# Performance work log

Measured on AMD Instinct MI355X. Metric: run time of the kernel, lower is better.

Reference implementation:

```python
import jax, jax.numpy as jnp
import numpy as np

GAMMA = 0.05      # train_config['loss']['gamma']
WARP = 256.0      # train_config['loss']['warp']
LAMBDA = 2.0      # train_config['loss']['lambda']
KL_START = 2000
KL_END = 8000
KL_UPPER = 1.0
BIG = 1e8  # stand-in for +inf that keeps softmin gradients finite


def kl_anneal(step):
    if step < KL_START:
        return 0.0
    elif step >= KL_END:
        return KL_UPPER
    else:
        return KL_UPPER * ((step - KL_START) / (KL_END - KL_START))


def _soft_dtw(x, y, gamma, warp):
    """Batched soft-DTW with warp penalty, anti-diagonal wavefront scan.
    x: (B, N, C), y: (B, M, C). Returns (B,) alignment costs R[N, M]."""
    B, N, C = x.shape
    M = y.shape[1]
    # squared Euclidean pairwise distance via GEMM (no (B,N,M,C) intermediate)
    x2 = jnp.sum(x * x, -1)
    y2 = jnp.sum(y * y, -1)
    D = x2[:, :, None] + y2[:, None, :] - 2.0 * jnp.einsum('bnc,bmc->bnm', x, y)  # (B,N,M)

    # precompute anti-diagonals of D: d = i + j runs 2..N+M, i runs 1..N, j = d - i
    ds = jnp.arange(2, N + M + 1)                      # (ND,) ND = N+M-1
    ii = jnp.arange(1, N + 1)                          # (N,)
    jj = ds[:, None] - ii[None, :]                     # (ND, N)
    valid = (jj >= 1) & (jj <= M)                      # (ND, N)
    Dg = D[:, (ii - 1)[None, :], jnp.clip(jj - 1, 0, M - 1)]  # (B, ND, N)
    Dg = jnp.where(valid[None], Dg, 0.0)
    Dg = jnp.transpose(Dg, (1, 0, 2))                  # (ND, B, N)

    # carry two previous R diagonals, each indexed by i = 0..N
    two = jnp.full((B, N + 1), BIG, x.dtype).at[:, 0].set(0.0)  # d = 0: R[0,0] = 0
    one = jnp.full((B, N + 1), BIG, x.dtype)                    # d = 1: all inf
    big_col = jnp.full((B, 1), BIG, x.dtype)

    def step(carry, inp):
        two, one = carry
        Dd, vld = inp                      # (B, N), (N,)
        diag = two[:, :-1]                 # R[i-1, j-1]
        up = one[:, :-1] + warp            # R[i-1, j] + warp
        left = one[:, 1:] + warp           # R[i, j-1] + warp
        s = jnp.stack([diag, up, left], 0)
        sm = -gamma * jax.nn.logsumexp(-s / gamma, axis=0)  # soft-min
        row = jnp.where(vld[None, :], Dd + sm, BIG)          # i = 1..N
        new = jnp.concatenate([big_col, row], axis=1)        # i = 0 row is inf
        return (one, new), None

    (_, last), _ = jax.lax.scan(step, (two, one), (Dg, valid))
    return last[:, N]  # R[N, M]


def setup_inputs() -> dict:
    key = jax.random.key(0)
    ks = jax.random.split(key, 7)
    K, B, T, C, S, Z = 4, 8, 800, 80, 128, 32
    return {
        "mel_iters": jax.random.normal(ks[0], (K, B, T, C), jnp.float32),
        "mel_targets": jax.random.normal(ks[1], (B, T, C), jnp.float32),
        "mel_lens_targets": jax.random.randint(ks[2], (B,), 100, T, jnp.int32),
        "src_lens_targets": jax.random.randint(ks[3], (B,), 50, S, jnp.int32),
        "durations": jax.random.uniform(ks[4], (B, S), jnp.float32, 0.0, 6.0),
        "mus": jax.random.normal(ks[5], (B, Z), jnp.float32),
        "log_vars": jax.random.normal(ks[6], (B, Z), jnp.float32),
        "step": 5000,
    }


def reference(mel_iters, mel_targets, mel_lens_targets, src_lens_targets,
              durations, mus, log_vars, step):
    K, B, T, C = mel_iters.shape
    y = jax.nn.sigmoid(mel_targets)                       # (B, T, C)
    xs = jax.nn.sigmoid(mel_iters).reshape(K * B, T, C)
    ys = jnp.broadcast_to(y[None], (K, B, T, C)).reshape(K * B, T, C)
    d = _soft_dtw(xs, ys, GAMMA, WARP).reshape(K, B)      # (K, B)
    # torch: mel_iter_loss += sdtw(...).mean()  (scalar sum of per-iter batch means)
    mel_iter_loss = jnp.sum(jnp.mean(d, axis=1))
    mel_lens_f = mel_lens_targets.astype(jnp.float32)
    mel_loss = jnp.mean(mel_iter_loss / (K * mel_lens_f))

    dur_err = jnp.abs(jnp.sum(durations, -1) - mel_lens_f)
    duration_loss = LAMBDA * jnp.mean(dur_err / src_lens_targets.astype(jnp.float32))

    beta = jnp.asarray(kl_anneal(step), jnp.float32)
    kl_loss = -0.5 * jnp.sum(1.0 + log_vars - mus ** 2 - jnp.exp(log_vars))

    total_loss = mel_loss + duration_loss + beta * kl_loss
    return (total_loss, mel_loss, duration_loss, kl_loss, beta)
```

## Files before the change

### kernel.cpp

```cpp
#include <hip/hip_runtime.h>
#include <math.h>
#include <stdint.h>

constexpr int K_ = 4, B_ = 8, T_ = 800, C_ = 80, S_ = 128, Z_ = 32;
constexpr int KB_ = K_ * B_;
constexpr int TC_ = T_ * C_;

#define BIGV   1e8f
#define WARP_V 256.0f

constexpr int NU_   = 900;
constexpr int SLAB_ = NU_ * 800;

__device__ __forceinline__ float sigmoidf_(float v) {
    return 1.f / (1.f + __expf(-v));
}

__global__ void fill_edge(float* __restrict__ Dm) {
    int kb = blockIdx.x;
    int t = threadIdx.x;
    if (t < 184) {
        int i = 8 + t;
        Dm[(size_t)kb * SLAB_ + (size_t)((i >> 3) - 1) * 800 + i] = BIGV;
    }
}

__global__ __launch_bounds__(256) void gemm_band(const float* __restrict__ mel_iters,
                                                 const float* __restrict__ mel_targets,
                                                 float* __restrict__ Dm) {
    const int kb = blockIdx.z;
    const int b  = kb & 7;
    const int ti = blockIdx.y;
    const int tj = ti + (int)blockIdx.x - 2;
    if ((unsigned)tj > 12u) return;

    const float* __restrict__ Xb = mel_iters + (size_t)kb * TC_;
    const float* __restrict__ Yb = mel_targets + (size_t)b * TC_;

    __shared__ float smem[10880];
    __shared__ float x2s[64], y2s[64];
    float (*xa)[68] = (float(*)[68])smem;
    float (*ya)[68] = (float(*)[68])(smem + 5440);

    const int tid = threadIdx.x;
    const int tx = tid & 15, ty = tid >> 4;
    const int i0 = ti * 64, j0 = tj * 64;

    {
        const int row = tid & 63, seg = tid >> 6;
        const int gi = min(i0 + row, T_ - 1);
        const int gj = min(j0 + row, T_ - 1);
        const float4* Xr = (const float4*)(Xb + (size_t)gi * C_);
        const float4* Yr = (const float4*)(Yb + (size_t)gj * C_);
        #pragma unroll
        for (int m = 0; m < 5; ++m) {
            const int k4 = seg * 5 + m;
            float4 xv = Xr[k4], yv = Yr[k4];
            const int k = k4 * 4;
            xa[k + 0][row] = sigmoidf_(xv.x); xa[k + 1][row] = sigmoidf_(xv.y);
            xa[k + 2][row] = sigmoidf_(xv.z); xa[k + 3][row] = sigmoidf_(xv.w);
            ya[k + 0][row] = sigmoidf_(yv.x); ya[k + 1][row] = sigmoidf_(yv.y);
            ya[k + 2][row] = sigmoidf_(yv.z); ya[k + 3][row] = sigmoidf_(yv.w);
        }
    }
    __syncthreads();

    if (tid < 64) {
        float s = 0.f;
        for (int k = 0; k < C_; ++k) { float v = xa[k][tid]; s += v * v; }
        x2s[tid] = s;
    } else if (tid < 128) {
        float s = 0.f;
        for (int k = 0; k < C_; ++k) { float v = ya[k][tid - 64]; s += v * v; }
        y2s[tid - 64] = s;
    }

    float acc[4][4] = {};
    #pragma unroll 16
    for (int k = 0; k < C_; ++k) {
        float4 av = *(const float4*)&xa[k][ty * 4];
        float4 bv = *(const float4*)&ya[k][tx * 4];
        acc[0][0] += av.x * bv.x; acc[0][1] += av.x * bv.y; acc[0][2] += av.x * bv.z; acc[0][3] += av.x * bv.w;
        acc[1][0] += av.y * bv.x; acc[1][1] += av.y * bv.y; acc[1][2] += av.y * bv.z; acc[1][3] += av.y * bv.w;
        acc[2][0] += av.z * bv.x; acc[2][1] += av.z * bv.y; acc[2][2] += av.z * bv.z; acc[2][3] += av.z * bv.w;
        acc[3][0] += av.w * bv.x; acc[3][1] += av.w * bv.y; acc[3][2] += av.w * bv.z; acc[3][3] += av.w * bv.w;
    }
    __syncthreads();

    float xs2[4], ys2[4];
    #pragma unroll
    for (int r = 0; r < 4; ++r) xs2[r] = x2s[ty * 4 + r];
    #pragma unroll
    for (int c = 0; c < 4; ++c) ys2[c] = y2s[tx * 4 + c];

    float* Zt = smem;
    const int sb = ty >> 1;
    #pragma unroll
    for (int r = 0; r < 4; ++r)
        #pragma unroll
        for (int c = 0; c < 4; ++c)
            Zt[(4 * tx + c + sb) * 65 + (4 * ty + r)] = xs2[r] + ys2[c] - 2.f * acc[r][c];
    __syncthreads();

    const int w0 = tid >> 6;
    const int lane = tid & 63;
    const int iGlob = i0 + lane;
    const int sbl = lane >> 3;
    const bool iok = iGlob < T_;
    const size_t ub = (size_t)(j0 + 8 * ti) * 800 + iGlob;
    #pragma unroll
    for (int it = 0; it < 18; ++it) {
        int w = w0 + it * 4;
        if (w > 70) break;
        int jrel = w - sbl;
        if (iok && (unsigned)jrel < 64u && (j0 + jrel) < T_)
            Dm[(size_t)kb * SLAB_ + ub + (size_t)w * 800] = Zt[w * 65 + lane];
    }
}


#define DCELL2(aS,aA,aB,aC,aD,aW, bS,bA,bB,bC,bD,bW) \
  "v_min3_f32 v" #aS ", v" #aA ", v" #aB ", v" #aC "\n\t" \
  "v_min3_f32 v" #bS ", v" #bA ", v" #bB ", v" #bC "\n\t" \
  "v_add_f32 v" #aS ", v" #aS ", v" #aD "\n\t" \
  "v_add_f32 v" #bS ", v" #bS ", v" #bD "\n\t" \
  "v_add_f32 v" #aW ", %[wK], v" #aS "\n\t" \
  "v_add_f32 v" #bW ", %[wK], v" #bS "\n\t"

#define STEP_E(q0,q1,q2,q3,q4,q5,q6,q7,q8,q9,q10,q11,q12,q13,q14,q15) \
  DCELL2(82, 45, 48, 66, q0, 98,    90, 89, 73, 74, q8, 106) \
  DCELL2(83, 50, 98, 67, q1, 99,    91, 58, 106, 75, q9, 107) \
  DCELL2(84, 51, 99, 68, q2, 100,   92, 59, 107, 76, q10, 108) \
  DCELL2(85, 52, 100, 69, q3, 101,  93, 60, 108, 77, q11, 109) \
  DCELL2(86, 53, 101, 70, q4, 102,  94, 61, 109, 78, q12, 110) \
  DCELL2(87, 54, 102, 71, q5, 103,  95, 62, 110, 79, q13, 111) \
  DCELL2(88, 55, 103, 72, q6, 104,  96, 63, 111, 80, q14, 112) \
  DCELL2(89, 56, 104, 73, q7, 105,  97, 64, 112, 81, q15, 113)

#define STEP_O(q0,q1,q2,q3,q4,q5,q6,q7,q8,q9,q10,q11,q12,q13,q14,q15) \
  DCELL2(50, 47, 46, 98, q0, 66,    58, 57, 105, 106, q8, 74) \
  DCELL2(51, 82, 66, 99, q1, 67,    59, 90, 74, 107, q9, 75) \
  DCELL2(52, 83, 67, 100, q2, 68,   60, 91, 75, 108, q10, 76) \
  DCELL2(53, 84, 68, 101, q3, 69,   61, 92, 76, 109, q11, 77) \
  DCELL2(54, 85, 69, 102, q4, 70,   62, 93, 77, 110, q12, 78) \
  DCELL2(55, 86, 70, 103, q5, 71,   63, 94, 78, 111, q13, 79) \
  DCELL2(56, 87, 71, 104, q6, 72,   64, 95, 79, 112, q14, 80) \
  DCELL2(57, 88, 72, 105, q7, 73,   65, 96, 80, 113, q15, 81)

#define HO_E \
  "s_nop 1\n\t" \
  "v_mov_b32_dpp v43, v97 wave_shr:1 row_mask:0xf bank_mask:0xf bound_ctrl:0\n\t" \
  "v_cndmask_b32 v45, v43, v42, %[msk]\n\t" \
  "v_add_f32 v46, %[wK], v45\n\t"

#define HO_O \
  "s_nop 1\n\t" \
  "v_mov_b32_dpp v43, v65 wave_shr:1 row_mask:0xf bank_mask:0xf bound_ctrl:0\n\t" \
  "v_cndmask_b32 v47, v43, v42, %[msk]\n\t" \
  "v_add_f32 v48, %[wK], v47\n\t"

#define PREF(r0,r1,r2,r3,K) \
  "s_add_u32 %[st], %[su], " #K "\n\t" \
  "v_med3_i32 v43, %[st], %[vlo], %[vhi]\n\t" \
  "v_mad_u32_u24 v44, v43, %[c32], %[vl4]\n\t" \
  "global_load_dwordx4 " r0 ", v44, %[bp]\n\t" \
  "global_load_dwordx4 " r1 ", v44, %[bp] offset:16\n\t" \
  "global_load_dwordx4 " r2 ", v44, %[bp] offset:32\n\t" \
  "global_load_dwordx4 " r3 ", v44, %[bp] offset:48\n\t"

#define PREF0(K) PREF("v[114:117]","v[118:121]","v[122:125]","v[126:129]",K)
#define PREF1(K) PREF("v[130:133]","v[134:137]","v[138:141]","v[142:145]",K)
#define PREF2(K) PREF("v[146:149]","v[150:153]","v[154:157]","v[158:161]",K)
#define PREF3(K) PREF("v[162:165]","v[166:169]","v[170:173]","v[174:177]",K)
#define PREF4(K) PREF("v[178:181]","v[182:185]","v[186:189]","v[190:193]",K)
#define PREF5(K) PREF("v[194:197]","v[198:201]","v[202:205]","v[206:209]",K)
#define PREF6(K) PREF("v[210:213]","v[214:217]","v[218:221]","v[222:225]",K)
#define PREF7(K) PREF("v[226:229]","v[230:233]","v[234:237]","v[238:241]",K)

#define SLOT0 (114,115,116,117,118,119,120,121,122,123,124,125,126,127,128,129)
#define SLOT1 (130,131,132,133,134,135,136,137,138,139,140,141,142,143,144,145)
#define SLOT2 (146,147,148,149,150,151,152,153,154,155,156,157,158,159,160,161)
#define SLOT3 (162,163,164,165,166,167,168,169,170,171,172,173,174,175,176,177)
#define SLOT4 (178,179,180,181,182,183,184,185,186,187,188,189,190,191,192,193)
#define SLOT5 (194,195,196,197,198,199,200,201,202,203,204,205,206,207,208,209)
#define SLOT6 (210,211,212,213,214,215,216,217,218,219,220,221,222,223,224,225)
#define SLOT7 (226,227,228,229,230,231,232,233,234,235,236,237,238,239,240,241)

#define DTW_CALL(M, A) M A

#define MV(n) "v_mov_b32 v" #n ", v42\n\t"
#define W28 "s_waitcnt vmcnt(28)\n\t"

__global__ __launch_bounds__(64)
void dtw_wave_kernel(const float* __restrict__ Dm, float* __restrict__ dtwv) {
    const int kb = blockIdx.x;
    const int l  = threadIdx.x;
    const int lc = l < 49 ? l : 49;
    const float* __restrict__ Dd = Dm + (size_t)kb * SLAB_;

    const int ti_l = lc >> 2;
    const int Jlo = ti_l >= 2 ? 64 * (ti_l - 2) : 0;
    const int Jhi = min(799, 64 * ti_l + 191);
    const int lo_u = (Jlo == 0) ? (2 * lc) : (Jlo + 2 * lc + 1);
    const int hi_u = Jhi + 2 * lc + 1;
    const unsigned lofs4 = (unsigned)(lc << 6);

    float res;
    unsigned su_d, st_d;

    asm volatile(
        "v_mov_b32 v42, %[vbig]\n\t"
        MV(50) MV(51) MV(52) MV(53) MV(54) MV(55) MV(56) MV(57)
        MV(58) MV(59) MV(60) MV(61) MV(62) MV(63) MV(64) MV(65)
        MV(66) MV(67) MV(68) MV(69) MV(70) MV(71) MV(72) MV(73)
        MV(74) MV(75) MV(76) MV(77) MV(78) MV(79) MV(80) MV(81)
        MV(82) MV(83) MV(84) MV(85) MV(86) MV(87) MV(88) MV(89)
        MV(90) MV(91) MV(92) MV(93) MV(94) MV(95) MV(96) MV(97)
        MV(98) MV(99) MV(100) MV(101) MV(102) MV(103) MV(104) MV(105)
        MV(106) MV(107) MV(108) MV(109) MV(110) MV(111) MV(112) MV(113)
        "v_cndmask_b32 v45, v42, 0, %[msk]\n\t"
        "v_mov_b32 v46, v42\n\t"
        "v_mov_b32 v47, v42\n\t"
        "v_mov_b32 v48, v42\n\t"
        "s_mov_b32 %[su], 0\n\t"
        PREF0(0) PREF1(1) PREF2(2) PREF3(3) PREF4(4) PREF5(5) PREF6(6) PREF7(7)
        "1:\n\t"
        W28 DTW_CALL(STEP_E, SLOT0) HO_E PREF0(8)
        W28 DTW_CALL(STEP_O, SLOT1) HO_O PREF1(9)
        W28 DTW_CALL(STEP_E, SLOT2) HO_E PREF2(10)
        W28 DTW_CALL(STEP_O, SLOT3) HO_O PREF3(11)
        W28 DTW_CALL(STEP_E, SLOT4) HO_E PREF4(12)
        W28 DTW_CALL(STEP_O, SLOT5) HO_O PREF5(13)
        W28 DTW_CALL(STEP_E, SLOT6) HO_E PREF6(14)
        W28 DTW_CALL(STEP_O, SLOT7) HO_O PREF7(15)
        "s_add_u32 %[su], %[su], 8\n\t"
        "s_cmp_lg_u32 %[su], 888\n\t"
        "s_cbranch_scc1 1b\n\t"
        W28 DTW_CALL(STEP_E, SLOT0) HO_E PREF0(8)
        W28 DTW_CALL(STEP_O, SLOT1) HO_O PREF1(9)
        W28 DTW_CALL(STEP_E, SLOT2) HO_E PREF2(10)
        W28 DTW_CALL(STEP_O, SLOT3) HO_O
        "s_waitcnt vmcnt(24)\n\t" DTW_CALL(STEP_E, SLOT4) HO_E
        "s_waitcnt vmcnt(20)\n\t" DTW_CALL(STEP_O, SLOT5) HO_O
        "s_waitcnt vmcnt(16)\n\t" DTW_CALL(STEP_E, SLOT6) HO_E
        "s_waitcnt vmcnt(12)\n\t" DTW_CALL(STEP_O, SLOT7) HO_O
        "s_waitcnt vmcnt(8)\n\t"  DTW_CALL(STEP_E, SLOT0) HO_E
        "s_waitcnt vmcnt(4)\n\t"  DTW_CALL(STEP_O, SLOT1) HO_O
        "s_waitcnt vmcnt(0)\n\t"  DTW_CALL(STEP_E, SLOT2)
        "v_mov_b32 %[res], v97\n\t"
        : [res] "=v"(res), [su] "=&s"(su_d), [st] "=&s"(st_d)
        : [vlo] "v"(lo_u), [vhi] "v"(hi_u), [vl4] "v"(lofs4),
          [vbig] "v"(BIGV), [wK] "s"(WARP_V), [c32] "s"(3200u),
          [msk] "s"(1ull), [bp] "s"((const void*)Dd)
        : "memory", "scc",
          "v42","v43","v44","v45","v46","v47","v48","v49",
          "v50","v51","v52","v53","v54","v55","v56","v57","v58","v59",
          "v60","v61","v62","v63","v64","v65","v66","v67","v68","v69",
          "v70","v71","v72","v73","v74","v75","v76","v77","v78","v79",
          "v80","v81","v82","v83","v84","v85","v86","v87","v88","v89",
          "v90","v91","v92","v93","v94","v95","v96","v97","v98","v99",
          "v100","v101","v102","v103","v104","v105","v106","v107","v108","v109",
          "v110","v111","v112","v113","v114","v115","v116","v117","v118","v119",
          "v120","v121","v122","v123","v124","v125","v126","v127","v128","v129",
          "v130","v131","v132","v133","v134","v135","v136","v137","v138","v139",
          "v140","v141","v142","v143","v144","v145","v146","v147","v148","v149",
          "v150","v151","v152","v153","v154","v155","v156","v157","v158","v159",
          "v160","v161","v162","v163","v164","v165","v166","v167","v168","v169",
          "v170","v171","v172","v173","v174","v175","v176","v177","v178","v179",
          "v180","v181","v182","v183","v184","v185","v186","v187","v188","v189",
          "v190","v191","v192","v193","v194","v195","v196","v197","v198","v199",
          "v200","v201","v202","v203","v204","v205","v206","v207","v208","v209",
          "v210","v211","v212","v213","v214","v215","v216","v217","v218","v219",
          "v220","v221","v222","v223","v224","v225","v226","v227","v228","v229",
          "v230","v231","v232","v233","v234","v235","v236","v237","v238","v239",
          "v240","v241"
    );

    if (l == 49) dtwv[kb] = res;
}

__global__ void finalize_kernel(const float* __restrict__ dtwv, const int* __restrict__ mel_lens,
                                const int* __restrict__ src_lens, const float* __restrict__ durations,
                                const float* __restrict__ mus, const float* __restrict__ log_vars,
                                const int* __restrict__ step, float* __restrict__ out) {
    const int lane = threadIdx.x;

    float v = (lane < KB_) ? dtwv[lane] : 0.f;
    for (int o = 32; o; o >>= 1) v += __shfl_down(v, o);

    float w = (lane < B_) ? 1.f / (K_ * (float)mel_lens[lane]) : 0.f;
    for (int o = 32; o; o >>= 1) w += __shfl_down(w, o);

    float du = 0.f;
    if (lane < B_) {
        float s = 0.f;
        for (int j = 0; j < S_; ++j) s += durations[lane * S_ + j];
        du = fabsf(s - (float)mel_lens[lane]) / (float)src_lens[lane];
    }
    for (int o = 32; o; o >>= 1) du += __shfl_down(du, o);

    float kl = 0.f;
    for (int j = lane; j < B_ * Z_; j += 64) {
        float muv = mus[j], lv = log_vars[j];
        kl += 1.f + lv - muv * muv - expf(lv);
    }
    for (int o = 32; o; o >>= 1) kl += __shfl_down(kl, o);

    if (lane == 0) {
        float mel_iter_loss = v / (float)B_;
        float mel_loss = mel_iter_loss * (w / (float)B_);
        float dur_loss = 2.0f * du / (float)B_;
        float kl_loss = -0.5f * kl;
        int st = step[0];
        float beta = (st < 2000) ? 0.f : ((st >= 8000) ? 1.f : (float)(st - 2000) / 6000.f);
        out[0] = mel_loss + dur_loss + beta * kl_loss;
        out[1] = mel_loss;
        out[2] = dur_loss;
        out[3] = kl_loss;
        out[4] = beta;
    }
}

extern "C" void kernel_launch(void* const* d_in, const int* in_sizes, int n_in,
                              void* d_out, int out_size, void* d_ws, size_t ws_size,
                              hipStream_t stream) {
    const float* mel_iters   = (const float*)d_in[0];
    const float* mel_targets = (const float*)d_in[1];
    const int*   mel_lens    = (const int*)d_in[2];
    const int*   src_lens    = (const int*)d_in[3];
    const float* durations   = (const float*)d_in[4];
    const float* mus         = (const float*)d_in[5];
    const float* log_vars    = (const float*)d_in[6];
    const int*   step        = (const int*)d_in[7];
    float* out = (float*)d_out;

    float* ws   = (float*)d_ws;
    float* Dm   = ws;
    float* dtwv = Dm + (size_t)KB_ * SLAB_;

    fill_edge<<<KB_, 192, 0, stream>>>(Dm);

    gemm_band<<<dim3(5, 13, KB_), 256, 0, stream>>>(mel_iters, mel_targets, Dm);

    dtw_wave_kernel<<<KB_, 64, 0, stream>>>(Dm, dtwv);

    finalize_kernel<<<1, 64, 0, stream>>>(dtwv, mel_lens, src_lens, durations, mus, log_vars, step, out);
}
```

Measured before the change: 213.7 us.

## Change skewed DTW slab layout and regroup wavefront cells for more ILP

The skew of the precomputed distance slab changes so that lanes own rows offset by 4 per lane instead of 2. The slab grows to 999 steps, and the edge-fill and GEMM store indexing are rewritten to match. The DTW asm step now interleaves four independent cell chains instead of two. This is meant to hide the min3/add latency of the serial wavefront with more independent instructions. In exchange the scan runs more steps (984 vs 888 loop bound) and the slab footprint grows.

```diff
diff --git a/kernel.cpp b/kernel.cpp
--- a/kernel.cpp
+++ b/kernel.cpp
@@ -9,7 +9,7 @@
 #define BIGV   1e8f
 #define WARP_V 256.0f
 
-constexpr int NU_   = 900;
+constexpr int NU_   = 999;
 constexpr int SLAB_ = NU_ * 800;
 
 __device__ __forceinline__ float sigmoidf_(float v) {
@@ -18,10 +18,18 @@
 
 __global__ void fill_edge(float* __restrict__ Dm) {
     int kb = blockIdx.x;
-    int t = threadIdx.x;
-    if (t < 184) {
-        int i = 8 + t;
-        Dm[(size_t)kb * SLAB_ + (size_t)((i >> 3) - 1) * 800 + i] = BIGV;
+    #pragma unroll
+    for (int m = 0; m < 5; ++m) {
+        int idx = threadIdx.x + 256 * m;
+        if (idx >= 1200) break;
+        int blk = idx / 24, rem = idx % 24;
+        int row, k;
+        if (rem < 4)       { row = 4 + rem;                 k = 1; }
+        else if (rem < 12) { int e = rem - 4;  row = 8 + (e >> 1);  k = 1 + (e & 1); }
+        else               { int e = rem - 12; row = 12 + e / 3;    k = 1 + e % 3; }
+        int i = 16 * blk + row;
+        int u = 4 * blk + (row >> 2) - k;
+        Dm[(size_t)kb * SLAB_ + (size_t)u * 800 + i] = BIGV;
     }
 }
 
@@ -94,7 +102,7 @@
     for (int c = 0; c < 4; ++c) ys2[c] = y2s[tx * 4 + c];
 
     float* Zt = smem;
-    const int sb = ty >> 1;
+    const int sb = ty;
     #pragma unroll
     for (int r = 0; r < 4; ++r)
         #pragma unroll
@@ -105,13 +113,13 @@
     const int w0 = tid >> 6;
     const int lane = tid & 63;
     const int iGlob = i0 + lane;
-    const int sbl = lane >> 3;
+    const int sbl = lane >> 2;
     const bool iok = iGlob < T_;
-    const size_t ub = (size_t)(j0 + 8 * ti) * 800 + iGlob;
-    #pragma unroll
-    for (int it = 0; it < 18; ++it) {
+    const size_t ub = (size_t)(j0 + 16 * ti) * 800 + iGlob;
+    #pragma unroll
+    for (int it = 0; it < 20; ++it) {
         int w = w0 + it * 4;
-        if (w > 70) break;
+        if (w > 78) break;
         int jrel = w - sbl;
         if (iok && (unsigned)jrel < 64u && (j0 + jrel) < T_)
             Dm[(size_t)kb * SLAB_ + ub + (size_t)w * 800] = Zt[w * 65 + lane];
@@ -119,33 +127,31 @@
 }
 
 
-#define DCELL2(aS,aA,aB,aC,aD,aW, bS,bA,bB,bC,bD,bW) \
-  "v_min3_f32 v" #aS ", v" #aA ", v" #aB ", v" #aC "\n\t" \
-  "v_min3_f32 v" #bS ", v" #bA ", v" #bB ", v" #bC "\n\t" \
-  "v_add_f32 v" #aS ", v" #aS ", v" #aD "\n\t" \
-  "v_add_f32 v" #bS ", v" #bS ", v" #bD "\n\t" \
-  "v_add_f32 v" #aW ", %[wK], v" #aS "\n\t" \
-  "v_add_f32 v" #bW ", %[wK], v" #bS "\n\t"
+#define QUAD(s0,w0,d0,u0,l0,q0, s1,w1,d1,u1,l1,q1, s2,w2,d2,u2,l2,q2, s3,w3,d3,u3,l3,q3) \
+  "v_min3_f32 v" #s0 ", v" #d0 ", v" #u0 ", v" #l0 "\n\t" \
+  "v_min3_f32 v" #s1 ", v" #d1 ", v" #u1 ", v" #l1 "\n\t" \
+  "v_min3_f32 v" #s2 ", v" #d2 ", v" #u2 ", v" #l2 "\n\t" \
+  "v_min3_f32 v" #s3 ", v" #d3 ", v" #u3 ", v" #l3 "\n\t" \
+  "v_add_f32 v" #s0 ", v" #s0 ", v" #q0 "\n\t" \
+  "v_add_f32 v" #s1 ", v" #s1 ", v" #q1 "\n\t" \
+  "v_add_f32 v" #s2 ", v" #s2 ", v" #q2 "\n\t" \
+  "v_add_f32 v" #s3 ", v" #s3 ", v" #q3 "\n\t" \
+  "v_add_f32 v" #w0 ", %[wK], v" #s0 "\n\t" \
+  "v_add_f32 v" #w1 ", %[wK], v" #s1 "\n\t" \
+  "v_add_f32 v" #w2 ", %[wK], v" #s2 "\n\t" \
+  "v_add_f32 v" #w3 ", %[wK], v" #s3 "\n\t"
 
 #define STEP_E(q0,q1,q2,q3,q4,q5,q6,q7,q8,q9,q10,q11,q12,q13,q14,q15) \
-  DCELL2(82, 45, 48, 66, q0, 98,    90, 89, 73, 74, q8, 106) \
-  DCELL2(83, 50, 98, 67, q1, 99,    91, 58, 106, 75, q9, 107) \
-  DCELL2(84, 51, 99, 68, q2, 100,   92, 59, 107, 76, q10, 108) \
-  DCELL2(85, 52, 100, 69, q3, 101,  93, 60, 108, 77, q11, 109) \
-  DCELL2(86, 53, 101, 70, q4, 102,  94, 61, 109, 78, q12, 110) \
-  DCELL2(87, 54, 102, 71, q5, 103,  95, 62, 110, 79, q13, 111) \
-  DCELL2(88, 55, 103, 72, q6, 104,  96, 63, 111, 80, q14, 112) \
-  DCELL2(89, 56, 104, 73, q7, 105,  97, 64, 112, 81, q15, 113)
+  QUAD(82,98,45,48,66,q0,    86,102,85,69,70,q4,   90,106,89,73,74,q8,   94,110,93,77,78,q12) \
+  QUAD(83,99,50,98,67,q1,    87,103,54,102,71,q5,  91,107,58,106,75,q9,  95,111,62,110,79,q13) \
+  QUAD(84,100,51,99,68,q2,   88,104,55,103,72,q6,  92,108,59,107,76,q10, 96,112,63,111,80,q14) \
+  QUAD(85,101,52,100,69,q3,  89,105,56,104,73,q7,  93,109,60,108,77,q11, 97,113,64,112,81,q15)
 
 #define STEP_O(q0,q1,q2,q3,q4,q5,q6,q7,q8,q9,q10,q11,q12,q13,q14,q15) \
-  DCELL2(50, 47, 46, 98, q0, 66,    58, 57, 105, 106, q8, 74) \
-  DCELL2(51, 82, 66, 99, q1, 67,    59, 90, 74, 107, q9, 75) \
-  DCELL2(52, 83, 67, 100, q2, 68,   60, 91, 75, 108, q10, 76) \
-  DCELL2(53, 84, 68, 101, q3, 69,   61, 92, 76, 109, q11, 77) \
-  DCELL2(54, 85, 69, 102, q4, 70,   62, 93, 77, 110, q12, 78) \
-  DCELL2(55, 86, 70, 103, q5, 71,   63, 94, 78, 111, q13, 79) \
-  DCELL2(56, 87, 71, 104, q6, 72,   64, 95, 79, 112, q14, 80) \
-  DCELL2(57, 88, 72, 105, q7, 73,   65, 96, 80, 113, q15, 81)
+  QUAD(50,66,47,46,98,q0,    54,70,53,101,102,q4,  58,74,57,105,106,q8,  62,78,61,109,110,q12) \
+  QUAD(51,67,82,66,99,q1,    55,71,86,70,103,q5,   59,75,90,74,107,q9,   63,79,94,78,111,q13) \
+  QUAD(52,68,83,67,100,q2,   56,72,87,71,104,q6,   60,76,91,75,108,q10,  64,80,95,79,112,q14) \
+  QUAD(53,69,84,68,101,q3,   57,73,88,72,105,q7,   61,77,92,76,109,q11,  65,81,96,80,113,q15)
 
 #define HO_E \
   "s_nop 1\n\t" \
@@ -201,8 +207,8 @@
     const int ti_l = lc >> 2;
     const int Jlo = ti_l >= 2 ? 64 * (ti_l - 2) : 0;
     const int Jhi = min(799, 64 * ti_l + 191);
-    const int lo_u = (Jlo == 0) ? (2 * lc) : (Jlo + 2 * lc + 1);
-    const int hi_u = Jhi + 2 * lc + 1;
+    const int lo_u = (Jlo == 0) ? (4 * lc) : (Jlo + 4 * lc + 3);
+    const int hi_u = min(998, Jhi + 4 * lc + 3);
     const unsigned lofs4 = (unsigned)(lc << 6);
 
     float res;
@@ -234,19 +240,23 @@
         W28 DTW_CALL(STEP_E, SLOT6) HO_E PREF6(14)
         W28 DTW_CALL(STEP_O, SLOT7) HO_O PREF7(15)
         "s_add_u32 %[su], %[su], 8\n\t"
-        "s_cmp_lg_u32 %[su], 888\n\t"
+        "s_cmp_lg_u32 %[su], 984\n\t"
         "s_cbranch_scc1 1b\n\t"
         W28 DTW_CALL(STEP_E, SLOT0) HO_E PREF0(8)
         W28 DTW_CALL(STEP_O, SLOT1) HO_O PREF1(9)
         W28 DTW_CALL(STEP_E, SLOT2) HO_E PREF2(10)
-        W28 DTW_CALL(STEP_O, SLOT3) HO_O
-        "s_waitcnt vmcnt(24)\n\t" DTW_CALL(STEP_E, SLOT4) HO_E
-        "s_waitcnt vmcnt(20)\n\t" DTW_CALL(STEP_O, SLOT5) HO_O
-        "s_waitcnt vmcnt(16)\n\t" DTW_CALL(STEP_E, SLOT6) HO_E
-        "s_waitcnt vmcnt(12)\n\t" DTW_CALL(STEP_O, SLOT7) HO_O
-        "s_waitcnt vmcnt(8)\n\t"  DTW_CALL(STEP_E, SLOT0) HO_E
-        "s_waitcnt vmcnt(4)\n\t"  DTW_CALL(STEP_O, SLOT1) HO_O
-        "s_waitcnt vmcnt(0)\n\t"  DTW_CALL(STEP_E, SLOT2)
+        W28 DTW_CALL(STEP_O, SLOT3) HO_O PREF3(11)
+        W28 DTW_CALL(STEP_E, SLOT4) HO_E PREF4(12)
+        W28 DTW_CALL(STEP_O, SLOT5) HO_O PREF5(13)
+        W28 DTW_CALL(STEP_E, SLOT6) HO_E PREF6(14)
+        W28 DTW_CALL(STEP_O, SLOT7) HO_O
+        "s_waitcnt vmcnt(24)\n\t" DTW_CALL(STEP_E, SLOT0) HO_E
+        "s_waitcnt vmcnt(20)\n\t" DTW_CALL(STEP_O, SLOT1) HO_O
+        "s_waitcnt vmcnt(16)\n\t" DTW_CALL(STEP_E, SLOT2) HO_E
+        "s_waitcnt vmcnt(12)\n\t" DTW_CALL(STEP_O, SLOT3) HO_O
+        "s_waitcnt vmcnt(8)\n\t"  DTW_CALL(STEP_E, SLOT4) HO_E
+        "s_waitcnt vmcnt(4)\n\t"  DTW_CALL(STEP_O, SLOT5) HO_O
+        "s_waitcnt vmcnt(0)\n\t"  DTW_CALL(STEP_E, SLOT6)
         "v_mov_b32 %[res], v97\n\t"
         : [res] "=v"(res), [su] "=&s"(su_d), [st] "=&s"(st_d)
         : [vlo] "v"(lo_u), [vhi] "v"(hi_u), [vl4] "v"(lofs4),
@@ -338,7 +348,7 @@
     float* Dm   = ws;
     float* dtwv = Dm + (size_t)KB_ * SLAB_;
 
-    fill_edge<<<KB_, 192, 0, stream>>>(Dm);
+    fill_edge<<<KB_, 256, 0, stream>>>(Dm);
 
     gemm_band<<<dim3(5, 13, KB_), 256, 0, stream>>>(mel_iters, mel_targets, Dm);
 
```

Result: slower. 223.5 us (+4.6%).

## Repack banded distance matrix into per-lane compact strips

Applied to the files above, without the earlier changes.

Changes the intermediate distance storage from a wide 900x800 skewed slab to per-lane strips of 336 rows by 16 floats. The GEMM writer computes strip-relative offsets and the DTW wavefront kernel's prefetch address math now clamps a relative index into each lane's strip. This shrinks the workspace footprint and makes each lane's loads contiguous, which should improve cache locality and cut wasted memory traffic. The risk is that the band bounds (336 rows) must exactly cover every lane's valid range.

```diff
diff --git a/kernel.cpp b/kernel.cpp
--- a/kernel.cpp
+++ b/kernel.cpp
@@ -9,8 +9,8 @@
 #define BIGV   1e8f
 #define WARP_V 256.0f
 
-constexpr int NU_   = 900;
-constexpr int SLAB_ = NU_ * 800;
+constexpr int STRF_ = 336 * 16;
+constexpr int SLAB_ = 50 * STRF_;
 
 __device__ __forceinline__ float sigmoidf_(float v) {
     return 1.f / (1.f + __expf(-v));
@@ -19,9 +19,10 @@
 __global__ void fill_edge(float* __restrict__ Dm) {
     int kb = blockIdx.x;
     int t = threadIdx.x;
-    if (t < 184) {
-        int i = 8 + t;
-        Dm[(size_t)kb * SLAB_ + (size_t)((i >> 3) - 1) * 800 + i] = BIGV;
+    if (t < 96) {
+        int lc = t >> 3;
+        int pos = 8 + (t & 7);
+        Dm[(size_t)kb * SLAB_ + (size_t)lc * STRF_ + pos] = BIGV;
     }
 }
 
@@ -107,14 +108,19 @@
     const int iGlob = i0 + lane;
     const int sbl = lane >> 3;
     const bool iok = iGlob < T_;
-    const size_t ub = (size_t)(j0 + 8 * ti) * 800 + iGlob;
+    const int lcS = 4 * ti + (lane >> 4);
+    const int JloS = ti >= 2 ? 64 * (ti - 2) : 0;
+    const int loS = (JloS == 0) ? (2 * lcS) : (JloS + 2 * lcS + 1);
+    const int tb = j0 + 8 * ti - loS;
+    float* lanePtr = Dm + (size_t)kb * SLAB_ + (size_t)lcS * STRF_ + (lane & 15);
     #pragma unroll
     for (int it = 0; it < 18; ++it) {
         int w = w0 + it * 4;
         if (w > 70) break;
         int jrel = w - sbl;
-        if (iok && (unsigned)jrel < 64u && (j0 + jrel) < T_)
-            Dm[(size_t)kb * SLAB_ + ub + (size_t)w * 800] = Zt[w * 65 + lane];
+        int tt = tb + w;
+        if (iok && (unsigned)jrel < 64u && (j0 + jrel) < T_ && (unsigned)tt < 336u)
+            lanePtr[(size_t)tt * 16] = Zt[w * 65 + lane];
     }
 }
 
@@ -161,8 +167,9 @@
 
 #define PREF(r0,r1,r2,r3,K) \
   "s_add_u32 %[st], %[su], " #K "\n\t" \
-  "v_med3_i32 v43, %[st], %[vlo], %[vhi]\n\t" \
-  "v_mad_u32_u24 v44, v43, %[c32], %[vl4]\n\t" \
+  "v_sub_u32 v43, %[st], %[vlo]\n\t" \
+  "v_med3_i32 v43, v43, 0, %[vlen]\n\t" \
+  "v_mad_u32_u24 v44, v43, 64, %[vbase]\n\t" \
   "global_load_dwordx4 " r0 ", v44, %[bp]\n\t" \
   "global_load_dwordx4 " r1 ", v44, %[bp] offset:16\n\t" \
   "global_load_dwordx4 " r2 ", v44, %[bp] offset:32\n\t" \
@@ -203,7 +210,8 @@
     const int Jhi = min(799, 64 * ti_l + 191);
     const int lo_u = (Jlo == 0) ? (2 * lc) : (Jlo + 2 * lc + 1);
     const int hi_u = Jhi + 2 * lc + 1;
-    const unsigned lofs4 = (unsigned)(lc << 6);
+    const int lenm1 = hi_u - lo_u;
+    const unsigned vbase = (unsigned)(lc * (STRF_ * 4));
 
     float res;
     unsigned su_d, st_d;
@@ -249,8 +257,8 @@
         "s_waitcnt vmcnt(0)\n\t"  DTW_CALL(STEP_E, SLOT2)
         "v_mov_b32 %[res], v97\n\t"
         : [res] "=v"(res), [su] "=&s"(su_d), [st] "=&s"(st_d)
-        : [vlo] "v"(lo_u), [vhi] "v"(hi_u), [vl4] "v"(lofs4),
-          [vbig] "v"(BIGV), [wK] "s"(WARP_V), [c32] "s"(3200u),
+        : [vlo] "v"(lo_u), [vlen] "v"(lenm1), [vbase] "v"(vbase),
+          [vbig] "v"(BIGV), [wK] "s"(WARP_V),
           [msk] "s"(1ull), [bp] "s"((const void*)Dd)
         : "memory", "scc",
           "v42","v43","v44","v45","v46","v47","v48","v49",
@@ -338,7 +346,7 @@
     float* Dm   = ws;
     float* dtwv = Dm + (size_t)KB_ * SLAB_;
 
-    fill_edge<<<KB_, 192, 0, stream>>>(Dm);
+    fill_edge<<<KB_, 96, 0, stream>>>(Dm);
 
     gemm_band<<<dim3(5, 13, KB_), 256, 0, stream>>>(mel_iters, mel_targets, Dm);
 
```

New measurement: 219.3 us. 1.03x slower.
